# Optimization experiments

Measured on AMD Instinct MI355X. Metric: run time of the kernel, lower is better.

The kernel has to match this reference:

```python
import jax, jax.numpy as jnp
import numpy as np

N_NODES = 50000
IN_FEATS, H_FEATS, OUT_FEATS = 128, 128, 40
N_EDGES = 800000


def gcn_conv(x, src, dst, deg_inv_sqrt, W, b):
    # PyG GCNConv (eval): h = x @ W; msg = norm * h[src]; out = scatter_add(msg -> dst) + b
    h = x @ W  # [N, F_out]
    norm = deg_inv_sqrt[src] * deg_inv_sqrt[dst]  # [E+N] (self-loops included)
    msg = h[src] * norm[:, None]
    out = jax.ops.segment_sum(msg, dst, num_segments=x.shape[0])
    return out + b


def setup_inputs() -> dict:
    key = jax.random.key(0)
    k1, k2, k3, k4 = jax.random.split(key, 4)
    x = jax.random.normal(k1, (N_NODES, IN_FEATS), dtype=jnp.float32)
    edge_index = jax.random.randint(k2, (2, N_EDGES), 0, N_NODES, dtype=jnp.int64)
    # Glorot-ish init for weights, zeros for bias (PyG default)
    W1 = jax.random.normal(k3, (IN_FEATS, H_FEATS), dtype=jnp.float32) / np.sqrt(IN_FEATS)
    b1 = jnp.zeros((H_FEATS,), dtype=jnp.float32)
    W2 = jax.random.normal(k4, (H_FEATS, OUT_FEATS), dtype=jnp.float32) / np.sqrt(H_FEATS)
    b2 = jnp.zeros((OUT_FEATS,), dtype=jnp.float32)
    return {"x": x, "edge_index": edge_index, "W1": W1, "b1": b1, "W2": W2, "b2": b2}


def reference(x, edge_index, W1, b1, W2, b2):
    n = x.shape[0]
    loop = jnp.arange(n, dtype=edge_index.dtype)
    src = jnp.concatenate([edge_index[0], loop])  # add self-loops
    dst = jnp.concatenate([edge_index[1], loop])
    # symmetric normalization: deg over destinations (incl. self-loops)
    deg = jnp.zeros((n,), dtype=x.dtype).at[dst].add(1.0)
    deg_inv_sqrt = jnp.where(deg > 0, jax.lax.rsqrt(deg), 0.0)
    # dropout(p=0.6) is identity in eval mode
    h = jax.nn.relu(gcn_conv(x, src, dst, deg_inv_sqrt, W1, b1))
    out = gcn_conv(h, src, dst, deg_inv_sqrt, W2, b2)
    return out
```

## Files before the change

### kernel.cpp

```cpp
#include <hip/hip_runtime.h>
#include <hip/hip_fp16.h>

#define THREADS 256
#define EPB 2048
#define LDK 136

using f16x8 = __attribute__((ext_vector_type(8))) _Float16;
using f32x4 = __attribute__((ext_vector_type(4))) float;


__global__ __launch_bounds__(256) void k_hist(const int* __restrict__ dst,
                                              int* __restrict__ Hmat,
                                              int e, int nbuck, int nbpad) {
    __shared__ int h[256];
    const int t = threadIdx.x;
    h[t] = 0;
    __syncthreads();
    const int base = blockIdx.x * EPB;
#pragma unroll
    for (int k = 0; k < 8; ++k) {
        int i = base + k * 256 + t;
        if (i < e) atomicAdd(&h[dst[i] >> 8], 1);
    }
    __syncthreads();
    if (t < nbuck) Hmat[t * nbpad + blockIdx.x] = h[t];
}

__global__ __launch_bounds__(256) void k_bscan(const int* __restrict__ Hmat,
                                               int* __restrict__ Off,
                                               int* __restrict__ btot,
                                               int nb, int nbpad) {
    __shared__ int s[256];
    const int b = blockIdx.x, t = threadIdx.x;
    const int* H = Hmat + b * nbpad;
    const int v0 = (2 * t     < nb) ? H[2 * t]     : 0;
    const int v1 = (2 * t + 1 < nb) ? H[2 * t + 1] : 0;
    const int p = v0 + v1;
    s[t] = p;
    __syncthreads();
    for (int off = 1; off < 256; off <<= 1) {
        int w = (t >= off) ? s[t - off] : 0;
        __syncthreads();
        s[t] += w;
        __syncthreads();
    }
    const int excl = s[t] - p;
    int* O = Off + b * nbpad;
    if (2 * t     < nb) O[2 * t]     = excl;
    if (2 * t + 1 < nb) O[2 * t + 1] = excl + v0;
    if (t == 255) btot[b] = s[255];
}

__global__ __launch_bounds__(256) void k_base(const int* __restrict__ btot,
                                              int* __restrict__ bbase,
                                              int* __restrict__ rowptr,
                                              int nbuck, int n, int e) {
    __shared__ int s[256];
    const int t = threadIdx.x;
    const int v = (t < nbuck) ? btot[t] : 0;
    s[t] = v;
    __syncthreads();
    for (int off = 1; off < 256; off <<= 1) {
        int w = (t >= off) ? s[t - off] : 0;
        __syncthreads();
        s[t] += w;
        __syncthreads();
    }
    if (t < nbuck) bbase[t] = s[t] - v;
    if (t == 0) { bbase[nbuck] = e; rowptr[n] = e; }
}

__global__ __launch_bounds__(256) void k_scat(const int* __restrict__ src,
                                              const int* __restrict__ dst,
                                              const int* __restrict__ Off,
                                              const int* __restrict__ bbase,
                                              int2* __restrict__ sorted,
                                              int e, int nbpad) {
    __shared__ int h[256];
    const int t = threadIdx.x;
    h[t] = 0;
    __syncthreads();
    const int base = blockIdx.x * EPB;
#pragma unroll
    for (int k = 0; k < 8; ++k) {
        int i = base + k * 256 + t;
        if (i < e) {
            const int d = dst[i];
            const int b = d >> 8;
            const int r = atomicAdd(&h[b], 1);
            const int pos = bbase[b] + Off[b * nbpad + blockIdx.x] + r;
            sorted[pos] = make_int2(src[i], d);
        }
    }
}

__global__ __launch_bounds__(256) void k_bsort(const int2* __restrict__ sorted,
                                               const int* __restrict__ bbase,
                                               int* __restrict__ csr_src,
                                               int* __restrict__ rowptr,
                                               float* __restrict__ dinv, int n) {
    __shared__ int cnt[256];
    __shared__ int s[256];
    __shared__ int fil[256];
    const int b = blockIdx.x, t = threadIdx.x;
    const int lo = bbase[b], hi = bbase[b + 1];
    cnt[t] = 0;
    __syncthreads();
    for (int p = lo + t; p < hi; p += 256) atomicAdd(&cnt[sorted[p].y & 255], 1);
    __syncthreads();
    const int c = cnt[t];
    s[t] = c;
    __syncthreads();
    for (int off = 1; off < 256; off <<= 1) {
        int w = (t >= off) ? s[t - off] : 0;
        __syncthreads();
        s[t] += w;
        __syncthreads();
    }
    const int excl = s[t] - c;
    const int node = b * 256 + t;
    if (node < n) {
        rowptr[node] = lo + excl;
        dinv[node] = rsqrtf((float)(c + 1));
    }
    fil[t] = lo + excl;
    __syncthreads();
    for (int p = lo + t; p < hi; p += 256) {
        const int2 pr = sorted[p];
        const int pos = atomicAdd(&fil[pr.y & 255], 1);
        csr_src[pos] = pr.x;
    }
}

__global__ __launch_bounds__(256) void k_gemm1(const float* __restrict__ x,
                                               const float* __restrict__ W,
                                               const float* __restrict__ dinv,
                                               __half* __restrict__ g, int n) {
    __shared__ _Float16 Wt[128 * LDK];
    __shared__ _Float16 xl[64 * LDK];
    const int t  = threadIdx.x;
    const int wv = t >> 6;
    const int l  = t & 63;
    const int base = blockIdx.x * 64;

#pragma unroll
    for (int i = 0; i < 64; ++i) {
        const int idx = t + 256 * i;
        const int nn = idx & 127, kk = idx >> 7;
        Wt[nn * LDK + kk] = (_Float16)W[kk * 128 + nn];
    }
#pragma unroll
    for (int i = 0; i < 8; ++i) {
        const int idx = t + 256 * i;
        const int r = idx >> 5, c4 = idx & 31;
        const int row = base + r;
        float4 v = make_float4(0.f, 0.f, 0.f, 0.f);
        if (row < n) v = *(const float4*)(x + (size_t)row * 128 + c4 * 4);
        _Float16* p = xl + r * LDK + c4 * 4;
        p[0] = (_Float16)v.x; p[1] = (_Float16)v.y;
        p[2] = (_Float16)v.z; p[3] = (_Float16)v.w;
    }
    __syncthreads();

    f32x4 acc[8];
#pragma unroll
    for (int i = 0; i < 8; ++i) acc[i] = (f32x4){0.f, 0.f, 0.f, 0.f};

    const int arow = wv * 16 + (l & 15);
    const int koff = (l >> 4) * 8;
#pragma unroll
    for (int kb = 0; kb < 4; ++kb) {
        const f16x8 a = *(const f16x8*)(xl + arow * LDK + kb * 32 + koff);
#pragma unroll
        for (int nt = 0; nt < 8; ++nt) {
            const f16x8 b = *(const f16x8*)(Wt + (nt * 16 + (l & 15)) * LDK + kb * 32 + koff);
            acc[nt] = __builtin_amdgcn_mfma_f32_16x16x32_f16(a, b, acc[nt], 0, 0, 0);
        }
    }

#pragma unroll
    for (int i = 0; i < 4; ++i) {
        const int row = base + wv * 16 + (l >> 4) * 4 + i;
        if (row < n) {
            const float dv = dinv[row];
#pragma unroll
            for (int nt = 0; nt < 8; ++nt)
                g[(size_t)row * 128 + nt * 16 + (l & 15)] = __float2half(acc[nt][i] * dv);
        }
    }
}

__global__ __launch_bounds__(256) void k_gather1(const __half2* __restrict__ g,
                                                 const int* __restrict__ rowptr,
                                                 const int* __restrict__ csr_src,
                                                 const float* __restrict__ dinv,
                                                 const float* __restrict__ b1,
                                                 __half2* __restrict__ out1, int n) {
    const int wave = threadIdx.x >> 6;
    const int lane = threadIdx.x & 63;
    const int d = blockIdx.x * 4 + wave;
    if (d >= n) return;
    const int beg = rowptr[d], end = rowptr[d + 1];
    float ax = 0.f, ay = 0.f, bx = 0.f, by = 0.f;
    int p = beg;
    for (; p + 4 <= end; p += 4) {
        const int s0 = csr_src[p],     s1 = csr_src[p + 1];
        const int s2 = csr_src[p + 2], s3 = csr_src[p + 3];
        const __half2 v0 = g[(size_t)s0 * 64 + lane];
        const __half2 v1 = g[(size_t)s1 * 64 + lane];
        const __half2 v2 = g[(size_t)s2 * 64 + lane];
        const __half2 v3 = g[(size_t)s3 * 64 + lane];
        const float2 f0 = __half22float2(v0), f1 = __half22float2(v1);
        const float2 f2 = __half22float2(v2), f3 = __half22float2(v3);
        ax += f0.x + f2.x; ay += f0.y + f2.y;
        bx += f1.x + f3.x; by += f1.y + f3.y;
    }
    for (; p < end; ++p) {
        const int s0 = csr_src[p];
        const float2 f0 = __half22float2(g[(size_t)s0 * 64 + lane]);
        ax += f0.x; ay += f0.y;
    }
    const float2 fs = __half22float2(g[(size_t)d * 64 + lane]);
    ax += bx + fs.x;
    ay += by + fs.y;
    const float dd = dinv[d];
    const float2 bb = *(const float2*)(b1 + lane * 2);
    const float rx = fmaxf(fmaf(dd, ax, bb.x), 0.f);
    const float ry = fmaxf(fmaf(dd, ay, bb.y), 0.f);
    out1[(size_t)d * 64 + lane] = __floats2half2_rn(rx, ry);
}

__global__ __launch_bounds__(256) void k_gemm2(const __half* __restrict__ h1,
                                               const float* __restrict__ W,
                                               const float* __restrict__ dinv,
                                               __half* __restrict__ g, int n) {
    __shared__ _Float16 Wt[48 * LDK];
    __shared__ _Float16 xl[64 * LDK];
    const int t  = threadIdx.x;
    const int wv = t >> 6;
    const int l  = t & 63;
    const int base = blockIdx.x * 64;

#pragma unroll
    for (int i = 0; i < 24; ++i) {
        const int idx = t + 256 * i;
        const int nn = idx % 48, kk = idx / 48;
        Wt[nn * LDK + kk] = (nn < 40) ? (_Float16)W[kk * 40 + nn] : (_Float16)0.f;
    }
#pragma unroll
    for (int i = 0; i < 4; ++i) {
        const int idx = t + 256 * i;
        const int r = idx >> 4, c8 = idx & 15;
        const int row = base + r;
        uint4 v = make_uint4(0u, 0u, 0u, 0u);
        if (row < n) v = *(const uint4*)(h1 + (size_t)row * 128 + c8 * 8);
        *(uint4*)(xl + r * LDK + c8 * 8) = v;
    }
    __syncthreads();

    f32x4 acc[3];
#pragma unroll
    for (int i = 0; i < 3; ++i) acc[i] = (f32x4){0.f, 0.f, 0.f, 0.f};

    const int arow = wv * 16 + (l & 15);
    const int koff = (l >> 4) * 8;
#pragma unroll
    for (int kb = 0; kb < 4; ++kb) {
        const f16x8 a = *(const f16x8*)(xl + arow * LDK + kb * 32 + koff);
#pragma unroll
        for (int nt = 0; nt < 3; ++nt) {
            const f16x8 b = *(const f16x8*)(Wt + (nt * 16 + (l & 15)) * LDK + kb * 32 + koff);
            acc[nt] = __builtin_amdgcn_mfma_f32_16x16x32_f16(a, b, acc[nt], 0, 0, 0);
        }
    }

#pragma unroll
    for (int i = 0; i < 4; ++i) {
        const int row = base + wv * 16 + (l >> 4) * 4 + i;
        if (row < n) {
            const float dv = dinv[row];
#pragma unroll
            for (int nt = 0; nt < 3; ++nt) {
                const int col = nt * 16 + (l & 15);
                if (col < 40)
                    g[(size_t)row * 40 + col] = __float2half(acc[nt][i] * dv);
            }
        }
    }
}

__global__ __launch_bounds__(256) void k_gather2(const __half2* __restrict__ g,
                                                 const int* __restrict__ rowptr,
                                                 const int* __restrict__ csr_src,
                                                 const float* __restrict__ dinv,
                                                 const float* __restrict__ b2,
                                                 float* __restrict__ out, int n) {
    const int wave = threadIdx.x >> 6;
    const int lane = threadIdx.x & 63;
    const int d = blockIdx.x * 4 + wave;
    if (d >= n) return;
    const int f  = lane & 31;
    const int eg = lane >> 5;
    const int fc = (f < 20) ? f : 19;
    const int beg = rowptr[d], end = rowptr[d + 1];
    float ax = 0.f, ay = 0.f;
    int p = beg + eg;
    for (; p + 2 < end; p += 4) {
        const int s0 = csr_src[p], s1 = csr_src[p + 2];
        const __half2 v0 = g[(size_t)s0 * 20 + fc];
        const __half2 v1 = g[(size_t)s1 * 20 + fc];
        const float2 f0 = __half22float2(v0), f1 = __half22float2(v1);
        ax += f0.x + f1.x;
        ay += f0.y + f1.y;
    }
    for (; p < end; p += 2) {
        const int s0 = csr_src[p];
        const float2 f0 = __half22float2(g[(size_t)s0 * 20 + fc]);
        ax += f0.x; ay += f0.y;
    }
    ax += __shfl_xor(ax, 32);
    ay += __shfl_xor(ay, 32);
    if (eg == 0 && f < 20) {
        const float2 fs = __half22float2(g[(size_t)d * 20 + f]);
        ax += fs.x; ay += fs.y;
        const float dd = dinv[d];
        const float2 bb = *(const float2*)(b2 + f * 2);
        float2 r;
        r.x = fmaf(dd, ax, bb.x);
        r.y = fmaf(dd, ay, bb.y);
        *(float2*)(out + (size_t)d * 40 + f * 2) = r;
    }
}

extern "C" void kernel_launch(void* const* d_in, const int* in_sizes, int n_in,
                              void* d_out, int out_size, void* d_ws, size_t ws_size,
                              hipStream_t stream) {
    const float* x  = (const float*)d_in[0];
    const int*   ei = (const int*)d_in[1];
    const float* W1 = (const float*)d_in[2];
    const float* b1 = (const float*)d_in[3];
    const float* W2 = (const float*)d_in[4];
    const float* b2 = (const float*)d_in[5];
    float* out = (float*)d_out;

    const int n = in_sizes[0] / 128;
    const int e = in_sizes[1] / 2;
    const int* src = ei;
    const int* dst = ei + e;

    const int n_pad = ((n + 63) / 64) * 64;
    const int e_pad = ((e + 63) / 64) * 64;
    const int NB    = (e + EPB - 1) / EPB;
    const int nbuck = (n + 255) >> 8;
    const int nbpad = ((NB + 63) / 64) * 64;

    float*   ws      = (float*)d_ws;
    float*   dinv    = ws;
    int*     rowptr  = (int*)(ws + n_pad);
    int*     csr_src = rowptr + n_pad + 64;
    __half2* g1      = (__half2*)(csr_src + e_pad);
    __half*  out1h   = (__half*)(g1 + (size_t)n_pad * 64);
    int2*    sorted  = (int2*)g1;
    int*     Hmat    = (int*)g1 + (size_t)e_pad * 2;
    int*     Off     = Hmat + nbuck * nbpad;
    int*     btot    = Off + nbuck * nbpad;
    int*     bbase   = btot + ((nbuck + 63) / 64) * 64;
    __half2* g2      = g1;

    const int nb_rows = (n + 63) / 64;
    const int nb_g    = (n + 3) / 4;

    k_hist <<<NB,    256, 0, stream>>>(dst, Hmat, e, nbuck, nbpad);
    k_bscan<<<nbuck, 256, 0, stream>>>(Hmat, Off, btot, NB, nbpad);
    k_base <<<1,     256, 0, stream>>>(btot, bbase, rowptr, nbuck, n, e);
    k_scat <<<NB,    256, 0, stream>>>(src, dst, Off, bbase, sorted, e, nbpad);
    k_bsort<<<nbuck, 256, 0, stream>>>(sorted, bbase, csr_src, rowptr, dinv, n);

    k_gemm1  <<<nb_rows, 256, 0, stream>>>(x, W1, dinv, (__half*)g1, n);
    k_gather1<<<nb_g, 256, 0, stream>>>(g1, rowptr, csr_src, dinv, b1, (__half2*)out1h, n);

    k_gemm2  <<<nb_rows, 256, 0, stream>>>(out1h, W2, dinv, (__half*)g2, n);
    k_gather2<<<nb_g, 256, 0, stream>>>(g2, rowptr, csr_src, dinv, b2, out, n);
}
```

Baseline: 136.9 us.

## Pre-convert weights, fold bucket-base scan into consumers, vectorize edge loads, retile gather2

```diff
diff --git a/kernel.cpp b/kernel.cpp
--- a/kernel.cpp
+++ b/kernel.cpp
@@ -7,6 +7,23 @@
 
 using f16x8 = __attribute__((ext_vector_type(8))) _Float16;
 using f32x4 = __attribute__((ext_vector_type(4))) float;
+
+__global__ __launch_bounds__(256) void k_wcvt(const float* __restrict__ W1,
+                                              const float* __restrict__ W2,
+                                              __half* __restrict__ wt1,
+                                              __half* __restrict__ wt2) {
+    const int idx = blockIdx.x * 256 + threadIdx.x;
+    if (idx < 128 * 128) {
+        const int nn = idx >> 7, kk = idx & 127;
+        wt1[idx] = __float2half(W1[kk * 128 + nn]);
+    } else {
+        const int o = idx - 128 * 128;
+        if (o < 48 * 128) {
+            const int nn = o >> 7, kk = o & 127;
+            wt2[o] = (nn < 40) ? __float2half(W2[kk * 40 + nn]) : __half(0.f);
+        }
+    }
+}
 
 
 __global__ __launch_bounds__(256) void k_hist(const int* __restrict__ dst,
@@ -16,11 +33,20 @@
     const int t = threadIdx.x;
     h[t] = 0;
     __syncthreads();
-    const int base = blockIdx.x * EPB;
-#pragma unroll
-    for (int k = 0; k < 8; ++k) {
-        int i = base + k * 256 + t;
-        if (i < e) atomicAdd(&h[dst[i] >> 8], 1);
+    const int base4 = blockIdx.x * 512;
+#pragma unroll
+    for (int k = 0; k < 2; ++k) {
+        const int i4 = base4 + k * 256 + t;
+        const int i = i4 * 4;
+        if (i + 3 < e) {
+            const int4 d4 = ((const int4*)dst)[i4];
+            atomicAdd(&h[d4.x >> 8], 1);
+            atomicAdd(&h[d4.y >> 8], 1);
+            atomicAdd(&h[d4.z >> 8], 1);
+            atomicAdd(&h[d4.w >> 8], 1);
+        } else {
+            for (int j = i; j < e; ++j) atomicAdd(&h[dst[j] >> 8], 1);
+        }
     }
     __syncthreads();
     if (t < nbuck) Hmat[t * nbpad + blockIdx.x] = h[t];
@@ -51,61 +77,88 @@
     if (t == 255) btot[b] = s[255];
 }
 
-__global__ __launch_bounds__(256) void k_base(const int* __restrict__ btot,
-                                              int* __restrict__ bbase,
-                                              int* __restrict__ rowptr,
-                                              int nbuck, int n, int e) {
-    __shared__ int s[256];
-    const int t = threadIdx.x;
-    const int v = (t < nbuck) ? btot[t] : 0;
-    s[t] = v;
-    __syncthreads();
-    for (int off = 1; off < 256; off <<= 1) {
-        int w = (t >= off) ? s[t - off] : 0;
-        __syncthreads();
-        s[t] += w;
-        __syncthreads();
-    }
-    if (t < nbuck) bbase[t] = s[t] - v;
-    if (t == 0) { bbase[nbuck] = e; rowptr[n] = e; }
-}
-
 __global__ __launch_bounds__(256) void k_scat(const int* __restrict__ src,
                                               const int* __restrict__ dst,
                                               const int* __restrict__ Off,
-                                              const int* __restrict__ bbase,
+                                              const int* __restrict__ btot,
                                               int2* __restrict__ sorted,
-                                              int e, int nbpad) {
+                                              int e, int nbuck, int nbpad) {
     __shared__ int h[256];
+    __shared__ int sc[256];
+    __shared__ int comb[256];
     const int t = threadIdx.x;
+    const int v = (t < nbuck) ? btot[t] : 0;
     h[t] = 0;
-    __syncthreads();
-    const int base = blockIdx.x * EPB;
-#pragma unroll
-    for (int k = 0; k < 8; ++k) {
-        int i = base + k * 256 + t;
-        if (i < e) {
-            const int d = dst[i];
-            const int b = d >> 8;
-            const int r = atomicAdd(&h[b], 1);
-            const int pos = bbase[b] + Off[b * nbpad + blockIdx.x] + r;
-            sorted[pos] = make_int2(src[i], d);
+    sc[t] = v;
+    __syncthreads();
+    for (int off = 1; off < 256; off <<= 1) {
+        int w = (t >= off) ? sc[t - off] : 0;
+        __syncthreads();
+        sc[t] += w;
+        __syncthreads();
+    }
+    comb[t] = (sc[t] - v) + ((t < nbuck) ? Off[t * nbpad + blockIdx.x] : 0);
+    __syncthreads();
+
+    const int base4 = blockIdx.x * 512;
+#pragma unroll
+    for (int k = 0; k < 2; ++k) {
+        const int i4 = base4 + k * 256 + t;
+        const int i = i4 * 4;
+        if (i + 3 < e) {
+            const int4 s4 = ((const int4*)src)[i4];
+            const int4 d4 = ((const int4*)dst)[i4];
+            {
+                const int b = d4.x >> 8;
+                sorted[comb[b] + atomicAdd(&h[b], 1)] = make_int2(s4.x, d4.x);
+            }
+            {
+                const int b = d4.y >> 8;
+                sorted[comb[b] + atomicAdd(&h[b], 1)] = make_int2(s4.y, d4.y);
+            }
+            {
+                const int b = d4.z >> 8;
+                sorted[comb[b] + atomicAdd(&h[b], 1)] = make_int2(s4.z, d4.z);
+            }
+            {
+                const int b = d4.w >> 8;
+                sorted[comb[b] + atomicAdd(&h[b], 1)] = make_int2(s4.w, d4.w);
+            }
+        } else {
+            for (int j = i; j < e; ++j) {
+                const int d = dst[j];
+                const int b = d >> 8;
+                sorted[comb[b] + atomicAdd(&h[b], 1)] = make_int2(src[j], d);
+            }
         }
     }
 }
 
 __global__ __launch_bounds__(256) void k_bsort(const int2* __restrict__ sorted,
-                                               const int* __restrict__ bbase,
+                                               const int* __restrict__ btot,
                                                int* __restrict__ csr_src,
                                                int* __restrict__ rowptr,
-                                               float* __restrict__ dinv, int n) {
+                                               float* __restrict__ dinv,
+                                               int n, int nbuck, int e) {
     __shared__ int cnt[256];
     __shared__ int s[256];
     __shared__ int fil[256];
     const int b = blockIdx.x, t = threadIdx.x;
-    const int lo = bbase[b], hi = bbase[b + 1];
+
+    const int v = (t < nbuck) ? btot[t] : 0;
+    s[t] = v;
     cnt[t] = 0;
     __syncthreads();
+    for (int off = 1; off < 256; off <<= 1) {
+        int w = (t >= off) ? s[t - off] : 0;
+        __syncthreads();
+        s[t] += w;
+        __syncthreads();
+    }
+    const int hi = s[b];
+    const int lo = hi - btot[b];
+    __syncthreads();
+
     for (int p = lo + t; p < hi; p += 256) atomicAdd(&cnt[sorted[p].y & 255], 1);
     __syncthreads();
     const int c = cnt[t];
@@ -123,6 +176,7 @@
         rowptr[node] = lo + excl;
         dinv[node] = rsqrtf((float)(c + 1));
     }
+    if (b == 0 && t == 0) rowptr[n] = e;
     fil[t] = lo + excl;
     __syncthreads();
     for (int p = lo + t; p < hi; p += 256) {
@@ -133,7 +187,7 @@
 }
 
 __global__ __launch_bounds__(256) void k_gemm1(const float* __restrict__ x,
-                                               const float* __restrict__ W,
+                                               const __half* __restrict__ wt1,
                                                const float* __restrict__ dinv,
                                                __half* __restrict__ g, int n) {
     __shared__ _Float16 Wt[128 * LDK];
@@ -143,11 +197,14 @@
     const int l  = t & 63;
     const int base = blockIdx.x * 64;
 
-#pragma unroll
-    for (int i = 0; i < 64; ++i) {
-        const int idx = t + 256 * i;
-        const int nn = idx & 127, kk = idx >> 7;
-        Wt[nn * LDK + kk] = (_Float16)W[kk * 128 + nn];
+    {
+        const uint4* Wg = (const uint4*)wt1;
+#pragma unroll
+        for (int i = 0; i < 8; ++i) {
+            const int idx = t + 256 * i;
+            const int row = idx >> 4, c8 = idx & 15;
+            *(uint4*)(Wt + row * LDK + c8 * 8) = Wg[idx];
+        }
     }
 #pragma unroll
     for (int i = 0; i < 8; ++i) {
@@ -156,9 +213,10 @@
         const int row = base + r;
         float4 v = make_float4(0.f, 0.f, 0.f, 0.f);
         if (row < n) v = *(const float4*)(x + (size_t)row * 128 + c4 * 4);
-        _Float16* p = xl + r * LDK + c4 * 4;
-        p[0] = (_Float16)v.x; p[1] = (_Float16)v.y;
-        p[2] = (_Float16)v.z; p[3] = (_Float16)v.w;
+        union { __half2 h2[2]; uint2 u; } pk;
+        pk.h2[0] = __floats2half2_rn(v.x, v.y);
+        pk.h2[1] = __floats2half2_rn(v.z, v.w);
+        *(uint2*)(xl + r * LDK + c4 * 4) = pk.u;
     }
     __syncthreads();
 
@@ -231,7 +289,7 @@
 }
 
 __global__ __launch_bounds__(256) void k_gemm2(const __half* __restrict__ h1,
-                                               const float* __restrict__ W,
+                                               const __half* __restrict__ wt2,
                                                const float* __restrict__ dinv,
                                                __half* __restrict__ g, int n) {
     __shared__ _Float16 Wt[48 * LDK];
@@ -241,11 +299,14 @@
     const int l  = t & 63;
     const int base = blockIdx.x * 64;
 
-#pragma unroll
-    for (int i = 0; i < 24; ++i) {
-        const int idx = t + 256 * i;
-        const int nn = idx % 48, kk = idx / 48;
-        Wt[nn * LDK + kk] = (nn < 40) ? (_Float16)W[kk * 40 + nn] : (_Float16)0.f;
+    {
+        const uint4* Wg = (const uint4*)wt2;
+#pragma unroll
+        for (int i = 0; i < 3; ++i) {
+            const int idx = t + 256 * i;
+            const int row = idx >> 4, c8 = idx & 15;
+            *(uint4*)(Wt + row * LDK + c8 * 8) = Wg[idx];
+        }
     }
 #pragma unroll
     for (int i = 0; i < 4; ++i) {
@@ -299,36 +360,28 @@
     const int lane = threadIdx.x & 63;
     const int d = blockIdx.x * 4 + wave;
     if (d >= n) return;
-    const int f  = lane & 31;
-    const int eg = lane >> 5;
-    const int fc = (f < 20) ? f : 19;
+    const int eg = lane / 20;
+    const int f  = lane - eg * 20;
     const int beg = rowptr[d], end = rowptr[d + 1];
     float ax = 0.f, ay = 0.f;
-    int p = beg + eg;
-    for (; p + 2 < end; p += 4) {
-        const int s0 = csr_src[p], s1 = csr_src[p + 2];
-        const __half2 v0 = g[(size_t)s0 * 20 + fc];
-        const __half2 v1 = g[(size_t)s1 * 20 + fc];
-        const float2 f0 = __half22float2(v0), f1 = __half22float2(v1);
-        ax += f0.x + f1.x;
-        ay += f0.y + f1.y;
-    }
-    for (; p < end; p += 2) {
-        const int s0 = csr_src[p];
-        const float2 f0 = __half22float2(g[(size_t)s0 * 20 + fc]);
-        ax += f0.x; ay += f0.y;
-    }
-    ax += __shfl_xor(ax, 32);
-    ay += __shfl_xor(ay, 32);
-    if (eg == 0 && f < 20) {
-        const float2 fs = __half22float2(g[(size_t)d * 20 + f]);
+    if (eg < 3) {
+        for (int p = beg + eg; p < end; p += 3) {
+            const int s0 = csr_src[p];
+            const float2 f0 = __half22float2(g[(size_t)s0 * 20 + f]);
+            ax += f0.x; ay += f0.y;
+        }
+    }
+    ax += __shfl(ax, lane + 20) + __shfl(ax, lane + 40);
+    ay += __shfl(ay, lane + 20) + __shfl(ay, lane + 40);
+    if (lane < 20) {
+        const float2 fs = __half22float2(g[(size_t)d * 20 + lane]);
         ax += fs.x; ay += fs.y;
         const float dd = dinv[d];
-        const float2 bb = *(const float2*)(b2 + f * 2);
+        const float2 bb = *(const float2*)(b2 + lane * 2);
         float2 r;
         r.x = fmaf(dd, ax, bb.x);
         r.y = fmaf(dd, ay, bb.y);
-        *(float2*)(out + (size_t)d * 40 + f * 2) = r;
+        *(float2*)(out + (size_t)d * 40 + lane * 2) = r;
     }
 }
 
@@ -360,25 +413,27 @@
     int*     csr_src = rowptr + n_pad + 64;
     __half2* g1      = (__half2*)(csr_src + e_pad);
     __half*  out1h   = (__half*)(g1 + (size_t)n_pad * 64);
+    __half*  wt1h    = out1h + (size_t)n_pad * 128;
+    __half*  wt2h    = wt1h + 128 * 128;
     int2*    sorted  = (int2*)g1;
     int*     Hmat    = (int*)g1 + (size_t)e_pad * 2;
     int*     Off     = Hmat + nbuck * nbpad;
     int*     btot    = Off + nbuck * nbpad;
-    int*     bbase   = btot + ((nbuck + 63) / 64) * 64;
     __half2* g2      = g1;
 
     const int nb_rows = (n + 63) / 64;
     const int nb_g    = (n + 3) / 4;
 
+    k_wcvt<<<(128 * 128 + 48 * 128 + 255) / 256, 256, 0, stream>>>(W1, W2, wt1h, wt2h);
+
     k_hist <<<NB,    256, 0, stream>>>(dst, Hmat, e, nbuck, nbpad);
     k_bscan<<<nbuck, 256, 0, stream>>>(Hmat, Off, btot, NB, nbpad);
-    k_base <<<1,     256, 0, stream>>>(btot, bbase, rowptr, nbuck, n, e);
-    k_scat <<<NB,    256, 0, stream>>>(src, dst, Off, bbase, sorted, e, nbpad);
-    k_bsort<<<nbuck, 256, 0, stream>>>(sorted, bbase, csr_src, rowptr, dinv, n);
-
-    k_gemm1  <<<nb_rows, 256, 0, stream>>>(x, W1, dinv, (__half*)g1, n);
+    k_scat <<<NB,    256, 0, stream>>>(src, dst, Off, btot, sorted, e, nbuck, nbpad);
+    k_bsort<<<nbuck, 256, 0, stream>>>(sorted, btot, csr_src, rowptr, dinv, n, nbuck, e);
+
+    k_gemm1  <<<nb_rows, 256, 0, stream>>>(x, wt1h, dinv, (__half*)g1, n);
     k_gather1<<<nb_g, 256, 0, stream>>>(g1, rowptr, csr_src, dinv, b1, (__half2*)out1h, n);
 
-    k_gemm2  <<<nb_rows, 256, 0, stream>>>(out1h, W2, dinv, (__half*)g2, n);
+    k_gemm2  <<<nb_rows, 256, 0, stream>>>(out1h, wt2h, dinv, (__half*)g2, n);
     k_gather2<<<nb_g, 256, 0, stream>>>(g2, rowptr, csr_src, dinv, b2, out, n);
 }
```

Result: faster. 130.4 us (-4.7%).
